# Performance work log

Measured on AMD Instinct MI355X. Metric: run time of the kernel, lower is better.

Reference implementation:

```python
import jax, jax.numpy as jnp
import numpy as np

B = 2_097_152   # batch
D = 64          # input_dim
H = 64          # num_hidden_units


def setup_inputs() -> dict:
    key = jax.random.key(0)
    kx, kw, kb = jax.random.split(key, 3)
    x = jax.random.normal(kx, (B, D), dtype=jnp.float32)
    # mlp[0] = nn.Linear(2*input_dim, num_hidden_units): weight [H, 2D], bias [H]
    W = jax.random.normal(kw, (H, 2 * D), dtype=jnp.float32) * 0.05
    b = jax.random.normal(kb, (H,), dtype=jnp.float32) * 0.05
    return {"x": x, "W": W, "b": b}


def reference(x, W, b):
    # HMSRL with num_layers=1: tree_structure = [(0, 0, 0, D)] -> single root node.
    # e is seeded with [x] (minimal fix: the original indexes an empty list).
    # left_child = e[0] = x; right index D >= len(e) -> right_child = zeros_like(x).
    # node_representation = mlp[0](cat(x, zeros)) = Linear(2D -> H).
    # cat(x, zeros) @ W.T == x @ W[:, :D].T, so skip materializing the zero half.
    return x @ W[:, :D].T + b
```

## Files before the change

### kernel.cpp

```cpp
#include <hip/hip_runtime.h>


#define ROWS_PER_TILE 8

__global__ __launch_bounds__(256, 4)
void hmsrl_kernel(const float* __restrict__ x, const float* __restrict__ W,
                  const float* __restrict__ b, float* __restrict__ out, int B) {
    __shared__ float xbuf[4][ROWS_PER_TILE * 64];

    const int lane = threadIdx.x & 63;
    const int wv   = threadIdx.x >> 6;

    const float4* wrow = reinterpret_cast<const float4*>(W + lane * 128);
    float4 wreg[16];
    #pragma unroll
    for (int j = 0; j < 16; ++j) wreg[j] = wrow[j];
    const float bias = b[lane];

    const int wave_global = blockIdx.x * 4 + wv;
    const int num_waves   = gridDim.x * 4;
    const int total_tiles = B / ROWS_PER_TILE;

    const float4* x4   = reinterpret_cast<const float4*>(x);
    float4* lbuf4      = reinterpret_cast<float4*>(xbuf[wv]);

    for (int tile = wave_global; tile < total_tiles; tile += num_waves) {
        const long base4 = (long)tile * 128;
        float4 v0 = x4[base4 + lane];
        float4 v1 = x4[base4 + 64 + lane];
        __syncthreads();
        lbuf4[lane]      = v0;
        lbuf4[64 + lane] = v1;
        __syncthreads();

        float acc[ROWS_PER_TILE];
        #pragma unroll
        for (int r = 0; r < ROWS_PER_TILE; ++r) acc[r] = bias;

        #pragma unroll
        for (int k4 = 0; k4 < 16; ++k4) {
            const float4 wvreg = wreg[k4];
            #pragma unroll
            for (int r = 0; r < ROWS_PER_TILE; ++r) {
                const float4 xv = lbuf4[r * 16 + k4];
                acc[r] = fmaf(xv.x, wvreg.x, acc[r]);
                acc[r] = fmaf(xv.y, wvreg.y, acc[r]);
                acc[r] = fmaf(xv.z, wvreg.z, acc[r]);
                acc[r] = fmaf(xv.w, wvreg.w, acc[r]);
            }
        }

        float* orow = out + (long)tile * (ROWS_PER_TILE * 64);
        #pragma unroll
        for (int r = 0; r < ROWS_PER_TILE; ++r) {
            orow[r * 64 + lane] = acc[r];
        }
    }
}

extern "C" void kernel_launch(void* const* d_in, const int* in_sizes, int n_in,
                              void* d_out, int out_size, void* d_ws, size_t ws_size,
                              hipStream_t stream) {
    const float* x = (const float*)d_in[0];
    const float* W = (const float*)d_in[1];
    const float* b = (const float*)d_in[2];
    float* out     = (float*)d_out;

    const int B = in_sizes[0] / 64;

    hmsrl_kernel<<<1024, 256, 0, stream>>>(x, W, b, out, B);
}
```

Baseline: 913.5 us.

## Stream x rows through scalar loads into SGPRs with prefetch, dropping LDS staging

```diff
diff --git a/kernel.cpp b/kernel.cpp
--- a/kernel.cpp
+++ b/kernel.cpp
@@ -1,60 +1,71 @@
 #include <hip/hip_runtime.h>
 
 
-#define ROWS_PER_TILE 8
+typedef __attribute__((ext_vector_type(16))) float f32x16;
+typedef __attribute__((ext_vector_type(4)))  float f32x4;
 
-__global__ __launch_bounds__(256, 4)
+#define WAVES_PER_BLOCK 4
+#define GRID_BLOCKS 1536
+
+__global__ __launch_bounds__(256, 6)
 void hmsrl_kernel(const float* __restrict__ x, const float* __restrict__ W,
                   const float* __restrict__ b, float* __restrict__ out, int B) {
-    __shared__ float xbuf[4][ROWS_PER_TILE * 64];
+    const int lane = threadIdx.x & 63;
 
-    const int lane = threadIdx.x & 63;
-    const int wv   = threadIdx.x >> 6;
-
-    const float4* wrow = reinterpret_cast<const float4*>(W + lane * 128);
-    float4 wreg[16];
+    const f32x4* wrow = reinterpret_cast<const f32x4*>(W + lane * 128);
+    f32x4 w[16];
     #pragma unroll
-    for (int j = 0; j < 16; ++j) wreg[j] = wrow[j];
+    for (int j = 0; j < 16; ++j) w[j] = wrow[j];
+    #pragma unroll
+    for (int j = 0; j < 16; ++j) asm volatile("" : "+v"(w[j]));
     const float bias = b[lane];
 
-    const int wave_global = blockIdx.x * 4 + wv;
-    const int num_waves   = gridDim.x * 4;
-    const int total_tiles = B / ROWS_PER_TILE;
+    int wid = blockIdx.x * WAVES_PER_BLOCK + (threadIdx.x >> 6);
+    wid = __builtin_amdgcn_readfirstlane(wid);
+    const int nw = gridDim.x * WAVES_PER_BLOCK;
 
-    const float4* x4   = reinterpret_cast<const float4*>(x);
-    float4* lbuf4      = reinterpret_cast<float4*>(xbuf[wv]);
+    const float* xp = x + (size_t)wid * 64;
+    float*       op = out + (size_t)wid * 64;
+    const size_t xstep = (size_t)nw * 64;
 
-    for (int tile = wave_global; tile < total_tiles; tile += num_waves) {
-        const long base4 = (long)tile * 128;
-        float4 v0 = x4[base4 + lane];
-        float4 v1 = x4[base4 + 64 + lane];
-        __syncthreads();
-        lbuf4[lane]      = v0;
-        lbuf4[64 + lane] = v1;
-        __syncthreads();
+    f32x16 c0, c1, c2, c3;
 
-        float acc[ROWS_PER_TILE];
+    asm volatile("s_load_dwordx16 %0, %1, 0x00" : "+s"(c0) : "s"(xp));
+    asm volatile("s_load_dwordx16 %0, %1, 0x40" : "+s"(c1) : "s"(xp));
+    asm volatile("s_load_dwordx16 %0, %1, 0x80" : "+s"(c2) : "s"(xp));
+    asm volatile("s_load_dwordx16 %0, %1, 0xc0" : "+s"(c3) : "s"(xp));
+
+    for (int row = wid; row < B; row += nw) {
+        const float* xn = (row + nw < B) ? (xp + xstep) : x;
+
+        asm volatile("s_waitcnt lgkmcnt(0)"
+                     : "+s"(c0), "+s"(c1), "+s"(c2), "+s"(c3));
+
+        float acc = bias;
         #pragma unroll
-        for (int r = 0; r < ROWS_PER_TILE; ++r) acc[r] = bias;
+        for (int j = 0; j < 16; ++j)
+            acc = fmaf(c0[j], w[j >> 2][j & 3], acc);
+        asm volatile("s_load_dwordx16 %0, %1, 0x00" : "+s"(c0) : "s"(xn));
 
         #pragma unroll
-        for (int k4 = 0; k4 < 16; ++k4) {
-            const float4 wvreg = wreg[k4];
-            #pragma unroll
-            for (int r = 0; r < ROWS_PER_TILE; ++r) {
-                const float4 xv = lbuf4[r * 16 + k4];
-                acc[r] = fmaf(xv.x, wvreg.x, acc[r]);
-                acc[r] = fmaf(xv.y, wvreg.y, acc[r]);
-                acc[r] = fmaf(xv.z, wvreg.z, acc[r]);
-                acc[r] = fmaf(xv.w, wvreg.w, acc[r]);
-            }
-        }
+        for (int j = 0; j < 16; ++j)
+            acc = fmaf(c1[j], w[4 + (j >> 2)][j & 3], acc);
+        asm volatile("s_load_dwordx16 %0, %1, 0x40" : "+s"(c1) : "s"(xn));
 
-        float* orow = out + (long)tile * (ROWS_PER_TILE * 64);
         #pragma unroll
-        for (int r = 0; r < ROWS_PER_TILE; ++r) {
-            orow[r * 64 + lane] = acc[r];
-        }
+        for (int j = 0; j < 16; ++j)
+            acc = fmaf(c2[j], w[8 + (j >> 2)][j & 3], acc);
+        asm volatile("s_load_dwordx16 %0, %1, 0x80" : "+s"(c2) : "s"(xn));
+
+        #pragma unroll
+        for (int j = 0; j < 16; ++j)
+            acc = fmaf(c3[j], w[12 + (j >> 2)][j & 3], acc);
+        asm volatile("s_load_dwordx16 %0, %1, 0xc0" : "+s"(c3) : "s"(xn));
+
+        op[lane] = acc;
+
+        xp = xn;
+        op += xstep;
     }
 }
 
@@ -68,5 +79,5 @@
 
     const int B = in_sizes[0] / 64;
 
-    hmsrl_kernel<<<1024, 256, 0, stream>>>(x, W, b, out, B);
+    hmsrl_kernel<<<GRID_BLOCKS, 256, 0, stream>>>(x, W, b, out, B);
 }
```

Measured after the change: 1.607 ms. 1.76x slower.
